# Kernel tuning notes

Measured on AMD Instinct MI355X. Metric: run time of the kernel, lower is better.

The kernel has to match this reference:

```python
import jax, jax.numpy as jnp
import numpy as np

B, T, F, H, M = 64, 512, 32, 512, 20
O = (F + 2) * M  # (n_features + 2) * num_mixtures = 680


def _lstm_cell(x, h, c, w_ih, w_hh, b_ih, b_hh):
    # torch.nn.LSTMCell: gates ordered [i, f, g, o]
    gates = x @ w_ih.T + h @ w_hh.T + b_ih + b_hh
    i, f, g, o = jnp.split(gates, 4, axis=-1)
    i = jax.nn.sigmoid(i)
    f = jax.nn.sigmoid(f)
    g = jnp.tanh(g)
    o = jax.nn.sigmoid(o)
    c_new = f * c + i * g
    h_new = o * jnp.tanh(c_new)
    return h_new, c_new


def setup_inputs() -> dict:
    key = jax.random.key(0)
    ks = jax.random.split(key, 9)
    s1 = 1.0 / np.sqrt(H)  # torch LSTMCell init: U(-1/sqrt(hidden), 1/sqrt(hidden))
    s2 = 1.0 / np.sqrt(O)
    u = lambda k, shape, s: jax.random.uniform(k, shape, jnp.float32, -s, s)
    return {
        "data": jax.random.normal(ks[0], (B, T * F), jnp.float32),
        "W_ih1": u(ks[1], (4 * H, F), s1),
        "W_hh1": u(ks[2], (4 * H, H), s1),
        "b_ih1": u(ks[3], (4 * H,), s1),
        "b_hh1": u(ks[4], (4 * H,), s1),
        "W_ih2": u(ks[5], (4 * O, H), s2),
        "W_hh2": u(ks[6], (4 * O, O), s2),
        "b_ih2": u(ks[7], (4 * O,), s2),
        "b_hh2": u(ks[8], (4 * O,), s2),
    }


def reference(data, W_ih1, W_hh1, b_ih1, b_hh1, W_ih2, W_hh2, b_ih2, b_hh2):
    n_feat = W_ih1.shape[1]
    hid = W_hh1.shape[1]
    out_dim = W_hh2.shape[1]
    batch = data.shape[0]
    t_steps = data.shape[1] // n_feat
    xs = data.reshape(batch, t_steps, n_feat).transpose(1, 0, 2)  # (T, B, F)

    h1 = jnp.zeros((batch, hid), data.dtype)
    c1 = jnp.zeros((batch, hid), data.dtype)
    h2 = jnp.zeros((batch, out_dim), data.dtype)
    c2 = jnp.zeros((batch, out_dim), data.dtype)

    def step(carry, x_t):
        h1, c1, h2, c2 = carry
        h1, c1 = _lstm_cell(x_t, h1, c1, W_ih1, W_hh1, b_ih1, b_hh1)
        # NOTE: original feeds lstm1's CELL state c1 into lstm2, and collects
        # lstm2's CELL state (`output`) as the per-step output.
        h2, c2 = _lstm_cell(c1, h2, c2, W_ih2, W_hh2, b_ih2, b_hh2)
        return (h1, c1, h2, c2), c2

    _, outs = jax.lax.scan(step, (h1, c1, h2, c2), xs)  # (T, B, O)
    return outs.transpose(1, 0, 2)  # (B, T, O), matches torch.stack(outputs, 1)
```

## Files before the change

### kernel.cpp

```cpp
#include <hip/hip_runtime.h>
#include <math.h>

#define BB 64
#define TT 512
#define FF 32
#define HH 512
#define OO 680

typedef _Float16 half8 __attribute__((ext_vector_type(8)));
typedef float f32x4 __attribute__((ext_vector_type(4)));

#define H1SLAB 65536u
#define C1SLAB 65536u
#define H2SLAB 90112u
#define H1S_OFF 0u
#define C1S_OFF 131072u
#define H2S_OFF 393216u
#define BAR_OFF 573440u
#define MEMSET_BYTES 576000u

#define L1B  16
#define NBLK 59
#define LDS_BYTES 155648u

#define L1CNT(g) ((g)*32)
#define L1FLG    64
#define L2CNT(g) (96 + (g)*32)
#define L2FLG    352

__device__ __forceinline__ float sigf(float x) { return 1.f / (1.f + expf(-x)); }

__device__ __forceinline__ unsigned long long aload8(const void* p) {
    return __hip_atomic_load((const unsigned long long*)p, __ATOMIC_RELAXED, __HIP_MEMORY_SCOPE_AGENT);
}
__device__ __forceinline__ void astore8(void* p, unsigned long long v) {
    __hip_atomic_store((unsigned long long*)p, v, __ATOMIC_RELAXED, __HIP_MEMORY_SCOPE_AGENT);
}
__device__ __forceinline__ void astore32(unsigned* p, unsigned v) {
    __hip_atomic_store(p, v, __ATOMIC_RELAXED, __HIP_MEMORY_SCOPE_AGENT);
}
__device__ __forceinline__ half8 ld_act(const char* p) {
    union { unsigned long long u[2]; half8 h; } t;
    t.u[0] = aload8(p); t.u[1] = aload8(p + 8);
    return t.h;
}
__device__ __forceinline__ unsigned pack2h(float a, float b) {
    union { _Float16 h[2]; unsigned u; } t;
    t.h[0] = (_Float16)a; t.h[1] = (_Float16)b; return t.u;
}
__device__ __forceinline__ unsigned long long pack4h(float a, float b, float c, float d) {
    union { _Float16 h[4]; unsigned long long u; } t;
    t.h[0] = (_Float16)a; t.h[1] = (_Float16)b; t.h[2] = (_Float16)c; t.h[3] = (_Float16)d;
    return t.u;
}
__device__ __forceinline__ unsigned minL1(const unsigned* bar) {
    const unsigned long long v = aload8(bar + L1FLG);
    const unsigned a = (unsigned)v, b = (unsigned)(v >> 32);
    return a < b ? a : b;
}
__device__ __forceinline__ unsigned minL2(const unsigned* bar) {
    const unsigned long long v0 = aload8(bar + L2FLG);
    const unsigned long long v1 = aload8(bar + L2FLG + 2);
    const unsigned long long v2 = aload8(bar + L2FLG + 4);
    const unsigned long long v3 = aload8(bar + L2FLG + 6);
    unsigned m = (unsigned)v0;
    unsigned x;
    x = (unsigned)(v0 >> 32); m = x < m ? x : m;
    x = (unsigned)v1;         m = x < m ? x : m;
    x = (unsigned)(v1 >> 32); m = x < m ? x : m;
    x = (unsigned)v2;         m = x < m ? x : m;
    x = (unsigned)(v2 >> 32); m = x < m ? x : m;
    x = (unsigned)v3;         m = x < m ? x : m;
    x = (unsigned)(v3 >> 32); m = x < m ? x : m;
    return m;
}

__global__ __launch_bounds__(256, 1)
void rnn_mfma(const float* __restrict__ data,
    const float* __restrict__ Wih1, const float* __restrict__ Whh1,
    const float* __restrict__ bih1, const float* __restrict__ bhh1,
    const float* __restrict__ Wih2, const float* __restrict__ Whh2,
    const float* __restrict__ bih2, const float* __restrict__ bhh2,
    char* __restrict__ wsb, float* __restrict__ out)
{
    extern __shared__ char lds[];
    const int tid = threadIdx.x, wv = tid >> 6, l = tid & 63;
    const int hi = l >> 4, lo = l & 15;
    const int blk = blockIdx.x;
    unsigned* bar = (unsigned*)(wsb + BAR_OFF);
    const int bfrag = wv;
    const int b = bfrag * 16 + lo;

    if (blk < L1B) {
        const int c0 = blk * 32;
        for (int u = tid; u < 136 * 256; u += 256) {
            const int tile = u >> 8, w = u & 255;
            const int ll = w >> 2, jj = w & 3;
            const int ks = tile >> 3, rest = tile & 7;
            const int gate = rest >> 1, chi = rest & 1;
            const int col = c0 + chi * 16 + (ll & 15);
            const int row = gate * HH + col;
            const int kk = ks * 32 + (ll >> 4) * 8 + jj * 2;
            const float v0 = (kk < FF)     ? Wih1[(size_t)row * FF + kk]     : Whh1[(size_t)row * HH + kk - FF];
            const float v1 = (kk + 1 < FF) ? Wih1[(size_t)row * FF + kk + 1] : Whh1[(size_t)row * HH + kk + 1 - FF];
            ((unsigned*)lds)[tile * 256 + w] = pack2h(v0, v1);
        }
        __syncthreads();

        float bs[2][4][4];
        #pragma unroll
        for (int chi = 0; chi < 2; ++chi)
            #pragma unroll
            for (int r = 0; r < 4; ++r) {
                const int col = c0 + chi * 16 + hi * 4 + r;
                #pragma unroll
                for (int g = 0; g < 4; ++g)
                    bs[chi][r][g] = bih1[g * HH + col] + bhh1[g * HH + col];
            }
        float cr[8] = {0.f,0.f,0.f,0.f,0.f,0.f,0.f,0.f};

        for (int s = 0; s < TT; ++s) {
            const int pr = s & 1;
            const float* xp = data + (size_t)b * (TT * FF) + (size_t)s * FF + hi * 8;
            const float4 xa = *(const float4*)xp;
            const float4 xb4 = *(const float4*)(xp + 4);
            if (s > 0) {
                if (tid == 0) { while (minL1(bar) < (unsigned)s) {} }
                __syncthreads();
            }
            half8 bx;
            bx[0] = (_Float16)xa.x; bx[1] = (_Float16)xa.y; bx[2] = (_Float16)xa.z; bx[3] = (_Float16)xa.w;
            bx[4] = (_Float16)xb4.x; bx[5] = (_Float16)xb4.y; bx[6] = (_Float16)xb4.z; bx[7] = (_Float16)xb4.w;

            f32x4 acc[8];
            #pragma unroll
            for (int a = 0; a < 8; ++a) acc[a] = (f32x4){0.f,0.f,0.f,0.f};
            #pragma unroll
            for (int a = 0; a < 8; ++a)
                acc[a] = __builtin_amdgcn_mfma_f32_16x16x32_f16(*(const half8*)(lds + (size_t)a * 1024 + (size_t)l * 16), bx, acc[a], 0, 0, 0);
            const char* h1p = wsb + H1S_OFF + (size_t)pr * H1SLAB + (size_t)l * 16;
            #pragma unroll
            for (int ks = 1; ks <= 16; ++ks) {
                const half8 bf = ld_act(h1p + (size_t)((ks - 1) * 4 + bfrag) * 1024);
                #pragma unroll
                for (int a = 0; a < 8; ++a)
                    acc[a] = __builtin_amdgcn_mfma_f32_16x16x32_f16(*(const half8*)(lds + (size_t)(ks * 8 + a) * 1024 + (size_t)l * 16), bf, acc[a], 0, 0, 0);
            }
            if (s > 3) {
                if (tid == 0) { while (minL2(bar) < (unsigned)(s - 3)) {} }
                __syncthreads();
            }
            char* h1w = wsb + H1S_OFF + (size_t)(pr ^ 1) * H1SLAB;
            char* c1w = wsb + C1S_OFF + (size_t)(s & 3) * C1SLAB;
            #pragma unroll
            for (int chi = 0; chi < 2; ++chi) {
                const int cc = c0 + chi * 16 + hi * 4;
                float cn[4], hn[4];
                #pragma unroll
                for (int r = 0; r < 4; ++r) {
                    const float ig = sigf(acc[0 + chi][r] + bs[chi][r][0]);
                    const float fg = sigf(acc[2 + chi][r] + bs[chi][r][1]);
                    const float gg = tanhf(acc[4 + chi][r] + bs[chi][r][2]);
                    const float og = sigf(acc[6 + chi][r] + bs[chi][r][3]);
                    const float c = fg * cr[chi * 4 + r] + ig * gg;
                    cr[chi * 4 + r] = c;
                    cn[r] = c; hn[r] = og * tanhf(c);
                }
                const size_t aoff = (size_t)((cc >> 5) * 4 + bfrag) * 1024
                                  + (size_t)((((cc >> 3) & 3) * 16 + lo)) * 16
                                  + (size_t)(cc & 7) * 2;
                astore8(h1w + aoff, pack4h(hn[0], hn[1], hn[2], hn[3]));
                astore8(c1w + aoff, pack4h(cn[0], cn[1], cn[2], cn[3]));
            }
            __syncthreads();
            if (tid == 0) {
                const int g = blk & 1;
                const unsigned e = (unsigned)(s + 1);
                const unsigned a2 = __hip_atomic_fetch_add(bar + L1CNT(g), 1u, __ATOMIC_RELAXED, __HIP_MEMORY_SCOPE_AGENT);
                if (a2 == e * 8u - 1u) astore32(bar + L1FLG + g, e);
            }
        }
    } else {
        const int idx = blk - L1B, c0 = idx * 16;
        const int grp = idx & 7;
        const unsigned gsz = (grp < 3) ? 6u : 5u;
        for (int u = tid; u < 152 * 256; u += 256) {
            const int tile = u >> 8, w = u & 255;
            const int ll = w >> 2, jj = w & 3;
            const int ks = tile >> 2, gate = tile & 3;
            const int col = c0 + (ll & 15);
            const int kk = ks * 32 + (ll >> 4) * 8 + jj * 2;
            float v0 = 0.f, v1 = 0.f;
            if (col < OO) {
                if (kk < HH) v0 = Wih2[((size_t)gate * OO + col) * HH + kk];
                else if (kk < 1192) v0 = Whh2[((size_t)gate * OO + col) * OO + kk - HH];
                if (kk + 1 < HH) v1 = Wih2[((size_t)gate * OO + col) * HH + kk + 1];
                else if (kk + 1 < 1192) v1 = Whh2[((size_t)gate * OO + col) * OO + kk + 1 - HH];
            }
            ((unsigned*)lds)[tile * 256 + w] = pack2h(v0, v1);
        }
        __syncthreads();

        const int cc = c0 + hi * 4;
        float bs[4][4];
        #pragma unroll
        for (int r = 0; r < 4; ++r) {
            const int col = cc + r;
            const bool ok = col < OO;
            #pragma unroll
            for (int g = 0; g < 4; ++g)
                bs[r][g] = ok ? (bih2[g * OO + col] + bhh2[g * OO + col]) : 0.f;
        }
        float cr[4] = {0.f,0.f,0.f,0.f};

        for (int t = 1; t <= TT; ++t) {
            if (tid == 0) { while (minL1(bar) < (unsigned)t) {} }
            __syncthreads();
            const char* c1p = wsb + C1S_OFF + (size_t)((t - 1) & 3) * C1SLAB + (size_t)l * 16;
            half8 bcs[16];
            #pragma unroll
            for (int ks = 0; ks < 16; ++ks) bcs[ks] = ld_act(c1p + (size_t)(ks * 4 + bfrag) * 1024);
            if (t > 1) {
                if (tid == 0) { while (minL2(bar) < (unsigned)(t - 1)) {} }
                __syncthreads();
            }
            const char* h2p = wsb + H2S_OFF + (size_t)((t & 1) ^ 1) * H2SLAB + (size_t)l * 16;
            half8 bhs[22];
            #pragma unroll
            for (int ks = 0; ks < 22; ++ks) bhs[ks] = ld_act(h2p + (size_t)(ks * 4 + bfrag) * 1024);
            f32x4 acc[4];
            #pragma unroll
            for (int g = 0; g < 4; ++g) acc[g] = (f32x4){0.f,0.f,0.f,0.f};
            #pragma unroll
            for (int ks = 0; ks < 16; ++ks) {
                #pragma unroll
                for (int g = 0; g < 4; ++g)
                    acc[g] = __builtin_amdgcn_mfma_f32_16x16x32_f16(*(const half8*)(lds + (size_t)(ks * 4 + g) * 1024 + (size_t)l * 16), bcs[ks], acc[g], 0, 0, 0);
            }
            #pragma unroll
            for (int ks = 0; ks < 22; ++ks) {
                #pragma unroll
                for (int g = 0; g < 4; ++g)
                    acc[g] = __builtin_amdgcn_mfma_f32_16x16x32_f16(*(const half8*)(lds + (size_t)((16 + ks) * 4 + g) * 1024 + (size_t)l * 16), bhs[ks], acc[g], 0, 0, 0);
            }
            if (cc < OO) {
                const int u_ = t - 1;
                float cn[4], hn[4];
                #pragma unroll
                for (int r = 0; r < 4; ++r) {
                    const float ig = sigf(acc[0][r] + bs[r][0]);
                    const float fg = sigf(acc[1][r] + bs[r][1]);
                    const float gg = tanhf(acc[2][r] + bs[r][2]);
                    const float og = sigf(acc[3][r] + bs[r][3]);
                    const float c = fg * cr[r] + ig * gg;
                    cr[r] = c;
                    cn[r] = c; hn[r] = og * tanhf(c);
                }
                const f32x4 q = {cn[0], cn[1], cn[2], cn[3]};
                __builtin_nontemporal_store(q, (f32x4*)(out + (size_t)b * (TT * OO) + (size_t)u_ * OO + cc));
                char* h2w = wsb + H2S_OFF + (size_t)(t & 1) * H2SLAB;
                const size_t aoff = (size_t)((cc >> 5) * 4 + bfrag) * 1024
                                  + (size_t)((((cc >> 3) & 3) * 16 + lo)) * 16
                                  + (size_t)(cc & 7) * 2;
                astore8(h2w + aoff, pack4h(hn[0], hn[1], hn[2], hn[3]));
            }
            __syncthreads();
            if (t < TT && tid == 0) {
                const unsigned a2 = __hip_atomic_fetch_add(bar + L2CNT(grp), 1u, __ATOMIC_RELAXED, __HIP_MEMORY_SCOPE_AGENT);
                if (a2 == (unsigned)t * gsz - 1u) astore32(bar + L2FLG + grp, (unsigned)t);
            }
        }
    }
}

extern "C" void kernel_launch(void* const* d_in, const int* in_sizes, int n_in,
                              void* d_out, int out_size, void* d_ws, size_t ws_size,
                              hipStream_t stream)
{
    const float* data = (const float*)d_in[0];
    const float* Wih1 = (const float*)d_in[1];
    const float* Whh1 = (const float*)d_in[2];
    const float* bih1 = (const float*)d_in[3];
    const float* bhh1 = (const float*)d_in[4];
    const float* Wih2 = (const float*)d_in[5];
    const float* Whh2 = (const float*)d_in[6];
    const float* bih2 = (const float*)d_in[7];
    const float* bhh2 = (const float*)d_in[8];
    float* out = (float*)d_out;
    char* wsb  = (char*)d_ws;

    hipFuncSetAttribute((const void*)rnn_mfma, hipFuncAttributeMaxDynamicSharedMemorySize, (int)LDS_BYTES);
    hipMemsetAsync(wsb, 0, MEMSET_BYTES, stream);
    rnn_mfma<<<NBLK, 256, LDS_BYTES, stream>>>(data,
                                               Wih1, Whh1, bih1, bhh1,
                                               Wih2, Whh2, bih2, bhh2,
                                               wsb, out);
}
```

Baseline: 4.495 ms.

## Replace block-level flag barriers with per-wave counter polling and overlap input MFMAs

Each wave now bumps a per-group counter after its own stores drain, replacing the __syncthreads plus block-leader fetch-add that also published a group flag. Every wave polls all counters itself with s_sleep backoff, so no block-wide barrier is needed. The input-projection MFMAs (x for layer 1, c1 for layer 2) are moved ahead of the dependency waits so they overlap the wait. This removes per-step block barriers and one level of flag indirection, at the cost of more polling traffic from every wave and a reliance on relaxed atomics plus waitcnt for ordering.

```diff
diff --git a/kernel.cpp b/kernel.cpp
--- a/kernel.cpp
+++ b/kernel.cpp
@@ -24,20 +24,18 @@
 #define LDS_BYTES 155648u
 
 #define L1CNT(g) ((g)*32)
-#define L1FLG    64
-#define L2CNT(g) (96 + (g)*32)
-#define L2FLG    352
+#define L2CNT(g) (64 + (g)*32)
 
 __device__ __forceinline__ float sigf(float x) { return 1.f / (1.f + expf(-x)); }
 
+__device__ __forceinline__ unsigned al32(const unsigned* p) {
+    return __hip_atomic_load(p, __ATOMIC_RELAXED, __HIP_MEMORY_SCOPE_AGENT);
+}
 __device__ __forceinline__ unsigned long long aload8(const void* p) {
     return __hip_atomic_load((const unsigned long long*)p, __ATOMIC_RELAXED, __HIP_MEMORY_SCOPE_AGENT);
 }
 __device__ __forceinline__ void astore8(void* p, unsigned long long v) {
     __hip_atomic_store((unsigned long long*)p, v, __ATOMIC_RELAXED, __HIP_MEMORY_SCOPE_AGENT);
-}
-__device__ __forceinline__ void astore32(unsigned* p, unsigned v) {
-    __hip_atomic_store(p, v, __ATOMIC_RELAXED, __HIP_MEMORY_SCOPE_AGENT);
 }
 __device__ __forceinline__ half8 ld_act(const char* p) {
     union { unsigned long long u[2]; half8 h; } t;
@@ -53,26 +51,25 @@
     t.h[0] = (_Float16)a; t.h[1] = (_Float16)b; t.h[2] = (_Float16)c; t.h[3] = (_Float16)d;
     return t.u;
 }
-__device__ __forceinline__ unsigned minL1(const unsigned* bar) {
-    const unsigned long long v = aload8(bar + L1FLG);
-    const unsigned a = (unsigned)v, b = (unsigned)(v >> 32);
-    return a < b ? a : b;
-}
-__device__ __forceinline__ unsigned minL2(const unsigned* bar) {
-    const unsigned long long v0 = aload8(bar + L2FLG);
-    const unsigned long long v1 = aload8(bar + L2FLG + 2);
-    const unsigned long long v2 = aload8(bar + L2FLG + 4);
-    const unsigned long long v3 = aload8(bar + L2FLG + 6);
-    unsigned m = (unsigned)v0;
-    unsigned x;
-    x = (unsigned)(v0 >> 32); m = x < m ? x : m;
-    x = (unsigned)v1;         m = x < m ? x : m;
-    x = (unsigned)(v1 >> 32); m = x < m ? x : m;
-    x = (unsigned)v2;         m = x < m ? x : m;
-    x = (unsigned)(v2 >> 32); m = x < m ? x : m;
-    x = (unsigned)v3;         m = x < m ? x : m;
-    x = (unsigned)(v3 >> 32); m = x < m ? x : m;
-    return m;
+
+__device__ __forceinline__ void wait2_ge(const unsigned* p0, const unsigned* p1, unsigned tgt) {
+    for (;;) {
+        const unsigned a = al32(p0), b = al32(p1);
+        if (a >= tgt && b >= tgt) return;
+        __builtin_amdgcn_s_sleep(1);
+    }
+}
+__device__ __forceinline__ bool l2done(const unsigned* bar, unsigned e) {
+    unsigned ok = 1u;
+    ok &= (al32(bar + L2CNT(0)) >= e * 24u);
+    ok &= (al32(bar + L2CNT(1)) >= e * 24u);
+    ok &= (al32(bar + L2CNT(2)) >= e * 24u);
+    ok &= (al32(bar + L2CNT(3)) >= e * 20u);
+    ok &= (al32(bar + L2CNT(4)) >= e * 20u);
+    ok &= (al32(bar + L2CNT(5)) >= e * 20u);
+    ok &= (al32(bar + L2CNT(6)) >= e * 20u);
+    ok &= (al32(bar + L2CNT(7)) >= e * 20u);
+    return ok != 0u;
 }
 
 __global__ __launch_bounds__(256, 1)
@@ -124,20 +121,18 @@
             const float* xp = data + (size_t)b * (TT * FF) + (size_t)s * FF + hi * 8;
             const float4 xa = *(const float4*)xp;
             const float4 xb4 = *(const float4*)(xp + 4);
-            if (s > 0) {
-                if (tid == 0) { while (minL1(bar) < (unsigned)s) {} }
-                __syncthreads();
-            }
             half8 bx;
             bx[0] = (_Float16)xa.x; bx[1] = (_Float16)xa.y; bx[2] = (_Float16)xa.z; bx[3] = (_Float16)xa.w;
             bx[4] = (_Float16)xb4.x; bx[5] = (_Float16)xb4.y; bx[6] = (_Float16)xb4.z; bx[7] = (_Float16)xb4.w;
-
             f32x4 acc[8];
             #pragma unroll
             for (int a = 0; a < 8; ++a) acc[a] = (f32x4){0.f,0.f,0.f,0.f};
             #pragma unroll
             for (int a = 0; a < 8; ++a)
                 acc[a] = __builtin_amdgcn_mfma_f32_16x16x32_f16(*(const half8*)(lds + (size_t)a * 1024 + (size_t)l * 16), bx, acc[a], 0, 0, 0);
+
+            if (s > 0) wait2_ge(bar + L1CNT(0), bar + L1CNT(1), (unsigned)s * 32u);
+
             const char* h1p = wsb + H1S_OFF + (size_t)pr * H1SLAB + (size_t)l * 16;
             #pragma unroll
             for (int ks = 1; ks <= 16; ++ks) {
@@ -147,8 +142,8 @@
                     acc[a] = __builtin_amdgcn_mfma_f32_16x16x32_f16(*(const half8*)(lds + (size_t)(ks * 8 + a) * 1024 + (size_t)l * 16), bf, acc[a], 0, 0, 0);
             }
             if (s > 3) {
-                if (tid == 0) { while (minL2(bar) < (unsigned)(s - 3)) {} }
-                __syncthreads();
+                const unsigned e = (unsigned)(s - 3);
+                while (!l2done(bar, e)) __builtin_amdgcn_s_sleep(8);
             }
             char* h1w = wsb + H1S_OFF + (size_t)(pr ^ 1) * H1SLAB;
             char* c1w = wsb + C1S_OFF + (size_t)(s & 3) * C1SLAB;
@@ -172,18 +167,13 @@
                 astore8(h1w + aoff, pack4h(hn[0], hn[1], hn[2], hn[3]));
                 astore8(c1w + aoff, pack4h(cn[0], cn[1], cn[2], cn[3]));
             }
-            __syncthreads();
-            if (tid == 0) {
-                const int g = blk & 1;
-                const unsigned e = (unsigned)(s + 1);
-                const unsigned a2 = __hip_atomic_fetch_add(bar + L1CNT(g), 1u, __ATOMIC_RELAXED, __HIP_MEMORY_SCOPE_AGENT);
-                if (a2 == e * 8u - 1u) astore32(bar + L1FLG + g, e);
-            }
+            __builtin_amdgcn_s_waitcnt(0);
+            if (l == 0)
+                __hip_atomic_fetch_add(bar + L1CNT(blk & 1), 1u, __ATOMIC_RELAXED, __HIP_MEMORY_SCOPE_AGENT);
         }
     } else {
         const int idx = blk - L1B, c0 = idx * 16;
         const int grp = idx & 7;
-        const unsigned gsz = (grp < 3) ? 6u : 5u;
         for (int u = tid; u < 152 * 256; u += 256) {
             const int tile = u >> 8, w = u & 255;
             const int ll = w >> 2, jj = w & 3;
@@ -214,29 +204,28 @@
         float cr[4] = {0.f,0.f,0.f,0.f};
 
         for (int t = 1; t <= TT; ++t) {
-            if (tid == 0) { while (minL1(bar) < (unsigned)t) {} }
-            __syncthreads();
+            wait2_ge(bar + L1CNT(0), bar + L1CNT(1), (unsigned)t * 32u);
             const char* c1p = wsb + C1S_OFF + (size_t)((t - 1) & 3) * C1SLAB + (size_t)l * 16;
             half8 bcs[16];
             #pragma unroll
             for (int ks = 0; ks < 16; ++ks) bcs[ks] = ld_act(c1p + (size_t)(ks * 4 + bfrag) * 1024);
-            if (t > 1) {
-                if (tid == 0) { while (minL2(bar) < (unsigned)(t - 1)) {} }
-                __syncthreads();
+            f32x4 acc[4];
+            #pragma unroll
+            for (int g = 0; g < 4; ++g) acc[g] = (f32x4){0.f,0.f,0.f,0.f};
+            #pragma unroll
+            for (int ks = 0; ks < 16; ++ks) {
+                #pragma unroll
+                for (int g = 0; g < 4; ++g)
+                    acc[g] = __builtin_amdgcn_mfma_f32_16x16x32_f16(*(const half8*)(lds + (size_t)(ks * 4 + g) * 1024 + (size_t)l * 16), bcs[ks], acc[g], 0, 0, 0);
+            }
+            {
+                const unsigned e = (unsigned)(t - 1);
+                while (!l2done(bar, e)) __builtin_amdgcn_s_sleep(1);
             }
             const char* h2p = wsb + H2S_OFF + (size_t)((t & 1) ^ 1) * H2SLAB + (size_t)l * 16;
             half8 bhs[22];
             #pragma unroll
             for (int ks = 0; ks < 22; ++ks) bhs[ks] = ld_act(h2p + (size_t)(ks * 4 + bfrag) * 1024);
-            f32x4 acc[4];
-            #pragma unroll
-            for (int g = 0; g < 4; ++g) acc[g] = (f32x4){0.f,0.f,0.f,0.f};
-            #pragma unroll
-            for (int ks = 0; ks < 16; ++ks) {
-                #pragma unroll
-                for (int g = 0; g < 4; ++g)
-                    acc[g] = __builtin_amdgcn_mfma_f32_16x16x32_f16(*(const half8*)(lds + (size_t)(ks * 4 + g) * 1024 + (size_t)l * 16), bcs[ks], acc[g], 0, 0, 0);
-            }
             #pragma unroll
             for (int ks = 0; ks < 22; ++ks) {
                 #pragma unroll
@@ -264,11 +253,9 @@
                                   + (size_t)(cc & 7) * 2;
                 astore8(h2w + aoff, pack4h(hn[0], hn[1], hn[2], hn[3]));
             }
-            __syncthreads();
-            if (t < TT && tid == 0) {
-                const unsigned a2 = __hip_atomic_fetch_add(bar + L2CNT(grp), 1u, __ATOMIC_RELAXED, __HIP_MEMORY_SCOPE_AGENT);
-                if (a2 == (unsigned)t * gsz - 1u) astore32(bar + L2FLG + grp, (unsigned)t);
-            }
+            __builtin_amdgcn_s_waitcnt(0);
+            if (t < TT && l == 0)
+                __hip_atomic_fetch_add(bar + L2CNT(grp), 1u, __ATOMIC_RELAXED, __HIP_MEMORY_SCOPE_AGENT);
         }
     }
 }
```

New measurement: 5.376 ms. +19.6%, slower.

## Merge LSTM1 and LSTM2 into uniform blocks with one shared barrier per step

Applied to the files above, without the earlier changes.

Replaces the split design (16 layer-1 blocks plus 43 layer-2 blocks with separate flags) with 64 identical blocks. Each block owns 8 layer-1 columns and 12 layer-2 columns with gate-interleaved weight tiles, and runs layer-1 step s alongside layer-2 step s-1 under a single grid barrier per step. The aim is to balance work and cut cross-group synchronisation latency on the serial recurrence. The cost is that every block now does both layers' MFMAs each step, and lane shuffles are needed to regroup gate outputs.

```diff
diff --git a/kernel.cpp b/kernel.cpp
--- a/kernel.cpp
+++ b/kernel.cpp
@@ -10,23 +10,18 @@
 typedef _Float16 half8 __attribute__((ext_vector_type(8)));
 typedef float f32x4 __attribute__((ext_vector_type(4)));
 
-#define H1SLAB 65536u
-#define C1SLAB 65536u
-#define H2SLAB 90112u
 #define H1S_OFF 0u
 #define C1S_OFF 131072u
-#define H2S_OFF 393216u
-#define BAR_OFF 573440u
-#define MEMSET_BYTES 576000u
-
-#define L1B  16
-#define NBLK 59
-#define LDS_BYTES 155648u
-
-#define L1CNT(g) ((g)*32)
-#define L1FLG    64
-#define L2CNT(g) (96 + (g)*32)
-#define L2FLG    352
+#define H2S_OFF 262144u
+#define BAR_OFF 442368u
+#define MEMSET_BYTES 443648u
+
+#define NBLK 64
+#define LDS_BYTES 151552u
+#define L2W_OFF 34816u
+
+#define CNT(g) ((g)*32)
+#define FLG    256
 
 __device__ __forceinline__ float sigf(float x) { return 1.f / (1.f + expf(-x)); }
 
@@ -53,18 +48,12 @@
     t.h[0] = (_Float16)a; t.h[1] = (_Float16)b; t.h[2] = (_Float16)c; t.h[3] = (_Float16)d;
     return t.u;
 }
-__device__ __forceinline__ unsigned minL1(const unsigned* bar) {
-    const unsigned long long v = aload8(bar + L1FLG);
-    const unsigned a = (unsigned)v, b = (unsigned)(v >> 32);
-    return a < b ? a : b;
-}
-__device__ __forceinline__ unsigned minL2(const unsigned* bar) {
-    const unsigned long long v0 = aload8(bar + L2FLG);
-    const unsigned long long v1 = aload8(bar + L2FLG + 2);
-    const unsigned long long v2 = aload8(bar + L2FLG + 4);
-    const unsigned long long v3 = aload8(bar + L2FLG + 6);
-    unsigned m = (unsigned)v0;
-    unsigned x;
+__device__ __forceinline__ unsigned minFlag(const unsigned* bar) {
+    const unsigned long long v0 = aload8(bar + FLG);
+    const unsigned long long v1 = aload8(bar + FLG + 2);
+    const unsigned long long v2 = aload8(bar + FLG + 4);
+    const unsigned long long v3 = aload8(bar + FLG + 6);
+    unsigned m = (unsigned)v0, x;
     x = (unsigned)(v0 >> 32); m = x < m ? x : m;
     x = (unsigned)v1;         m = x < m ? x : m;
     x = (unsigned)(v1 >> 32); m = x < m ? x : m;
@@ -74,9 +63,14 @@
     x = (unsigned)(v3 >> 32); m = x < m ? x : m;
     return m;
 }
+__device__ __forceinline__ size_t slab_waddr(int cc, int b) {
+    return (size_t)((cc >> 5) * 4 + (b >> 4)) * 1024
+         + (size_t)((((cc >> 3) & 3) * 16 + (b & 15))) * 16
+         + (size_t)(cc & 7) * 2;
+}
 
 __global__ __launch_bounds__(256, 1)
-void rnn_mfma(const float* __restrict__ data,
+void rnn_merged(const float* __restrict__ data,
     const float* __restrict__ Wih1, const float* __restrict__ Whh1,
     const float* __restrict__ bih1, const float* __restrict__ bhh1,
     const float* __restrict__ Wih2, const float* __restrict__ Whh2,
@@ -86,189 +80,179 @@
     extern __shared__ char lds[];
     const int tid = threadIdx.x, wv = tid >> 6, l = tid & 63;
     const int hi = l >> 4, lo = l & 15;
-    const int blk = blockIdx.x;
+    const int bk = blockIdx.x;
     unsigned* bar = (unsigned*)(wsb + BAR_OFF);
-    const int bfrag = wv;
-    const int b = bfrag * 16 + lo;
-
-    if (blk < L1B) {
-        const int c0 = blk * 32;
-        for (int u = tid; u < 136 * 256; u += 256) {
-            const int tile = u >> 8, w = u & 255;
-            const int ll = w >> 2, jj = w & 3;
-            const int ks = tile >> 3, rest = tile & 7;
-            const int gate = rest >> 1, chi = rest & 1;
-            const int col = c0 + chi * 16 + (ll & 15);
-            const int row = gate * HH + col;
-            const int kk = ks * 32 + (ll >> 4) * 8 + jj * 2;
-            const float v0 = (kk < FF)     ? Wih1[(size_t)row * FF + kk]     : Whh1[(size_t)row * HH + kk - FF];
-            const float v1 = (kk + 1 < FF) ? Wih1[(size_t)row * FF + kk + 1] : Whh1[(size_t)row * HH + kk + 1 - FF];
-            ((unsigned*)lds)[tile * 256 + w] = pack2h(v0, v1);
-        }
-        __syncthreads();
-
-        float bs[2][4][4];
+    const int b = wv * 16 + lo;
+
+    for (int u = tid; u < 34 * 256; u += 256) {
+        const int tt = u >> 8, w = u & 255;
+        const int ks = tt >> 1, q = tt & 1;
+        const int ll = w >> 2, jj = w & 3;
+        const int fq = q * 16 + (ll & 15);
+        const int col = bk * 8 + (fq >> 2);
+        const int gate = fq & 3;
+        const int grow = gate * HH + col;
+        const int k = ks * 32 + (ll >> 4) * 8 + jj * 2;
+        const float v0 = (k < FF)     ? Wih1[(size_t)grow * FF + k]     : Whh1[(size_t)grow * HH + k - FF];
+        const float v1 = (k + 1 < FF) ? Wih1[(size_t)grow * FF + k + 1] : Whh1[(size_t)grow * HH + k + 1 - FF];
+        ((unsigned*)lds)[tt * 256 + w] = pack2h(v0, v1);
+    }
+    for (int u = tid; u < 114 * 256; u += 256) {
+        const int tt = u >> 8, w = u & 255;
+        const int ks = tt / 3, q = tt - ks * 3;
+        const int ll = w >> 2, jj = w & 3;
+        const int fq = q * 16 + (ll & 15);
+        const int col = bk * 12 + (fq >> 2);
+        const int gate = fq & 3;
+        const int k = ks * 32 + (ll >> 4) * 8 + jj * 2;
+        float v0 = 0.f, v1 = 0.f;
+        if (col < OO) {
+            if (k < HH) v0 = Wih2[((size_t)gate * OO + col) * HH + k];
+            else if (k < 1192) v0 = Whh2[((size_t)gate * OO + col) * OO + k - HH];
+            if (k + 1 < HH) v1 = Wih2[((size_t)gate * OO + col) * HH + k + 1];
+            else if (k + 1 < 1192) v1 = Whh2[((size_t)gate * OO + col) * OO + k + 1 - HH];
+        }
+        ((unsigned*)(lds + L2W_OFF))[tt * 256 + w] = pack2h(v0, v1);
+    }
+    __syncthreads();
+
+    float bs1[2][4], bs2[3][4];
+    #pragma unroll
+    for (int q = 0; q < 2; ++q) {
+        const int col = bk * 8 + q * 4 + hi;
         #pragma unroll
-        for (int chi = 0; chi < 2; ++chi)
-            #pragma unroll
-            for (int r = 0; r < 4; ++r) {
-                const int col = c0 + chi * 16 + hi * 4 + r;
-                #pragma unroll
-                for (int g = 0; g < 4; ++g)
-                    bs[chi][r][g] = bih1[g * HH + col] + bhh1[g * HH + col];
-            }
-        float cr[8] = {0.f,0.f,0.f,0.f,0.f,0.f,0.f,0.f};
-
-        for (int s = 0; s < TT; ++s) {
-            const int pr = s & 1;
+        for (int g = 0; g < 4; ++g) bs1[q][g] = bih1[g * HH + col] + bhh1[g * HH + col];
+    }
+    #pragma unroll
+    for (int q = 0; q < 3; ++q) {
+        const int col = bk * 12 + q * 4 + hi;
+        const bool ok = col < OO;
+        #pragma unroll
+        for (int g = 0; g < 4; ++g) bs2[q][g] = ok ? (bih2[g * OO + col] + bhh2[g * OO + col]) : 0.f;
+    }
+    float cr1[2] = {0.f, 0.f};
+    float cr2[3] = {0.f, 0.f, 0.f};
+
+    for (int s = 0; s <= TT; ++s) {
+        const int wr = s & 1, rd = wr ^ 1;
+        f32x4 a10 = {0,0,0,0}, a11 = {0,0,0,0};
+        if (s < TT) {
             const float* xp = data + (size_t)b * (TT * FF) + (size_t)s * FF + hi * 8;
             const float4 xa = *(const float4*)xp;
             const float4 xb4 = *(const float4*)(xp + 4);
-            if (s > 0) {
-                if (tid == 0) { while (minL1(bar) < (unsigned)s) {} }
-                __syncthreads();
-            }
             half8 bx;
             bx[0] = (_Float16)xa.x; bx[1] = (_Float16)xa.y; bx[2] = (_Float16)xa.z; bx[3] = (_Float16)xa.w;
             bx[4] = (_Float16)xb4.x; bx[5] = (_Float16)xb4.y; bx[6] = (_Float16)xb4.z; bx[7] = (_Float16)xb4.w;
-
-            f32x4 acc[8];
-            #pragma unroll
-            for (int a = 0; a < 8; ++a) acc[a] = (f32x4){0.f,0.f,0.f,0.f};
-            #pragma unroll
-            for (int a = 0; a < 8; ++a)
-                acc[a] = __builtin_amdgcn_mfma_f32_16x16x32_f16(*(const half8*)(lds + (size_t)a * 1024 + (size_t)l * 16), bx, acc[a], 0, 0, 0);
-            const char* h1p = wsb + H1S_OFF + (size_t)pr * H1SLAB + (size_t)l * 16;
+            a10 = __builtin_amdgcn_mfma_f32_16x16x32_f16(*(const half8*)(lds + (size_t)l * 16), bx, a10, 0, 0, 0);
+            a11 = __builtin_amdgcn_mfma_f32_16x16x32_f16(*(const half8*)(lds + 1024 + (size_t)l * 16), bx, a11, 0, 0, 0);
+        }
+        if (s > 0) {
+            if (tid == 0) { while (minFlag(bar) < (unsigned)s) {} }
+            __syncthreads();
+        }
+        float pend[4]; float* pendP = nullptr;
+
+        if (s < TT) {
+            const char* h1p = wsb + H1S_OFF + (size_t)rd * 65536u + (size_t)l * 16;
+            half8 bh[16];
+            #pragma unroll
+            for (int ks = 0; ks < 16; ++ks) bh[ks] = ld_act(h1p + (size_t)(ks * 4 + wv) * 1024);
             #pragma unroll
             for (int ks = 1; ks <= 16; ++ks) {
-                const half8 bf = ld_act(h1p + (size_t)((ks - 1) * 4 + bfrag) * 1024);
-                #pragma unroll
-                for (int a = 0; a < 8; ++a)
-                    acc[a] = __builtin_amdgcn_mfma_f32_16x16x32_f16(*(const half8*)(lds + (size_t)(ks * 8 + a) * 1024 + (size_t)l * 16), bf, acc[a], 0, 0, 0);
-            }
-            if (s > 3) {
-                if (tid == 0) { while (minL2(bar) < (unsigned)(s - 3)) {} }
-                __syncthreads();
-            }
-            char* h1w = wsb + H1S_OFF + (size_t)(pr ^ 1) * H1SLAB;
-            char* c1w = wsb + C1S_OFF + (size_t)(s & 3) * C1SLAB;
-            #pragma unroll
-            for (int chi = 0; chi < 2; ++chi) {
-                const int cc = c0 + chi * 16 + hi * 4;
-                float cn[4], hn[4];
-                #pragma unroll
-                for (int r = 0; r < 4; ++r) {
-                    const float ig = sigf(acc[0 + chi][r] + bs[chi][r][0]);
-                    const float fg = sigf(acc[2 + chi][r] + bs[chi][r][1]);
-                    const float gg = tanhf(acc[4 + chi][r] + bs[chi][r][2]);
-                    const float og = sigf(acc[6 + chi][r] + bs[chi][r][3]);
-                    const float c = fg * cr[chi * 4 + r] + ig * gg;
-                    cr[chi * 4 + r] = c;
-                    cn[r] = c; hn[r] = og * tanhf(c);
+                a10 = __builtin_amdgcn_mfma_f32_16x16x32_f16(*(const half8*)(lds + (size_t)(ks * 2) * 1024 + (size_t)l * 16), bh[ks - 1], a10, 0, 0, 0);
+                a11 = __builtin_amdgcn_mfma_f32_16x16x32_f16(*(const half8*)(lds + (size_t)(ks * 2 + 1) * 1024 + (size_t)l * 16), bh[ks - 1], a11, 0, 0, 0);
+            }
+            float cn1[2], hn1[2];
+            #pragma unroll
+            for (int q = 0; q < 2; ++q) {
+                const f32x4 a = (q == 0) ? a10 : a11;
+                const float ig = sigf(a[0] + bs1[q][0]);
+                const float fg = sigf(a[1] + bs1[q][1]);
+                const float gg = tanhf(a[2] + bs1[q][2]);
+                const float og = sigf(a[3] + bs1[q][3]);
+                const float c = fg * cr1[q] + ig * gg;
+                cr1[q] = c;
+                cn1[q] = c; hn1[q] = og * tanhf(c);
+            }
+            char* h1w = wsb + H1S_OFF + (size_t)wr * 65536u;
+            char* c1w = wsb + C1S_OFF + (size_t)wr * 65536u;
+            #pragma unroll
+            for (int q = 0; q < 2; ++q) {
+                const float h0 = __shfl(hn1[q], lo), h1v = __shfl(hn1[q], 16 + lo);
+                const float h2v = __shfl(hn1[q], 32 + lo), h3 = __shfl(hn1[q], 48 + lo);
+                const float c0 = __shfl(cn1[q], lo), c1v = __shfl(cn1[q], 16 + lo);
+                const float c2v = __shfl(cn1[q], 32 + lo), c3 = __shfl(cn1[q], 48 + lo);
+                if (hi == q) {
+                    const int cc = bk * 8 + q * 4;
+                    const size_t ad = slab_waddr(cc, b);
+                    astore8(h1w + ad, pack4h(h0, h1v, h2v, h3));
+                    astore8(c1w + ad, pack4h(c0, c1v, c2v, c3));
                 }
-                const size_t aoff = (size_t)((cc >> 5) * 4 + bfrag) * 1024
-                                  + (size_t)((((cc >> 3) & 3) * 16 + lo)) * 16
-                                  + (size_t)(cc & 7) * 2;
-                astore8(h1w + aoff, pack4h(hn[0], hn[1], hn[2], hn[3]));
-                astore8(c1w + aoff, pack4h(cn[0], cn[1], cn[2], cn[3]));
-            }
-            __syncthreads();
-            if (tid == 0) {
-                const int g = blk & 1;
-                const unsigned e = (unsigned)(s + 1);
-                const unsigned a2 = __hip_atomic_fetch_add(bar + L1CNT(g), 1u, __ATOMIC_RELAXED, __HIP_MEMORY_SCOPE_AGENT);
-                if (a2 == e * 8u - 1u) astore32(bar + L1FLG + g, e);
-            }
-        }
-    } else {
-        const int idx = blk - L1B, c0 = idx * 16;
-        const int grp = idx & 7;
-        const unsigned gsz = (grp < 3) ? 6u : 5u;
-        for (int u = tid; u < 152 * 256; u += 256) {
-            const int tile = u >> 8, w = u & 255;
-            const int ll = w >> 2, jj = w & 3;
-            const int ks = tile >> 2, gate = tile & 3;
-            const int col = c0 + (ll & 15);
-            const int kk = ks * 32 + (ll >> 4) * 8 + jj * 2;
-            float v0 = 0.f, v1 = 0.f;
-            if (col < OO) {
-                if (kk < HH) v0 = Wih2[((size_t)gate * OO + col) * HH + kk];
-                else if (kk < 1192) v0 = Whh2[((size_t)gate * OO + col) * OO + kk - HH];
-                if (kk + 1 < HH) v1 = Wih2[((size_t)gate * OO + col) * HH + kk + 1];
-                else if (kk + 1 < 1192) v1 = Whh2[((size_t)gate * OO + col) * OO + kk + 1 - HH];
-            }
-            ((unsigned*)lds)[tile * 256 + w] = pack2h(v0, v1);
+            }
+        }
+        if (s >= 1) {
+            f32x4 a20 = {0,0,0,0}, a21 = {0,0,0,0}, a22 = {0,0,0,0};
+            const char* c1p = wsb + C1S_OFF + (size_t)rd * 65536u + (size_t)l * 16;
+            half8 bc[16];
+            #pragma unroll
+            for (int ks = 0; ks < 16; ++ks) bc[ks] = ld_act(c1p + (size_t)(ks * 4 + wv) * 1024);
+            #pragma unroll
+            for (int ks = 0; ks < 16; ++ks) {
+                const char* at = lds + L2W_OFF + (size_t)(ks * 3) * 1024 + (size_t)l * 16;
+                a20 = __builtin_amdgcn_mfma_f32_16x16x32_f16(*(const half8*)(at       ), bc[ks], a20, 0, 0, 0);
+                a21 = __builtin_amdgcn_mfma_f32_16x16x32_f16(*(const half8*)(at + 1024), bc[ks], a21, 0, 0, 0);
+                a22 = __builtin_amdgcn_mfma_f32_16x16x32_f16(*(const half8*)(at + 2048), bc[ks], a22, 0, 0, 0);
+            }
+            const char* h2p = wsb + H2S_OFF + (size_t)rd * 90112u + (size_t)l * 16;
+            half8 bh2[22];
+            #pragma unroll
+            for (int kk = 0; kk < 22; ++kk) bh2[kk] = ld_act(h2p + (size_t)(kk * 4 + wv) * 1024);
+            #pragma unroll
+            for (int kk = 0; kk < 22; ++kk) {
+                const char* at = lds + L2W_OFF + (size_t)((16 + kk) * 3) * 1024 + (size_t)l * 16;
+                a20 = __builtin_amdgcn_mfma_f32_16x16x32_f16(*(const half8*)(at       ), bh2[kk], a20, 0, 0, 0);
+                a21 = __builtin_amdgcn_mfma_f32_16x16x32_f16(*(const half8*)(at + 1024), bh2[kk], a21, 0, 0, 0);
+                a22 = __builtin_amdgcn_mfma_f32_16x16x32_f16(*(const half8*)(at + 2048), bh2[kk], a22, 0, 0, 0);
+            }
+            float cn2[3], hn2[3];
+            #pragma unroll
+            for (int q = 0; q < 3; ++q) {
+                const f32x4 a = (q == 0) ? a20 : (q == 1) ? a21 : a22;
+                const float ig = sigf(a[0] + bs2[q][0]);
+                const float fg = sigf(a[1] + bs2[q][1]);
+                const float gg = tanhf(a[2] + bs2[q][2]);
+                const float og = sigf(a[3] + bs2[q][3]);
+                const float c = fg * cr2[q] + ig * gg;
+                cr2[q] = c;
+                cn2[q] = c; hn2[q] = og * tanhf(c);
+            }
+            char* h2w = wsb + H2S_OFF + (size_t)wr * 90112u;
+            #pragma unroll
+            for (int q = 0; q < 3; ++q) {
+                const float h0 = __shfl(hn2[q], lo), h1v = __shfl(hn2[q], 16 + lo);
+                const float h2v = __shfl(hn2[q], 32 + lo), h3 = __shfl(hn2[q], 48 + lo);
+                const float c0 = __shfl(cn2[q], lo), c1v = __shfl(cn2[q], 16 + lo);
+                const float c2v = __shfl(cn2[q], 32 + lo), c3 = __shfl(cn2[q], 48 + lo);
+                if (hi == q) {
+                    const int cc = bk * 12 + q * 4;
+                    if (cc + 4 <= OO) {
+                        astore8(h2w + slab_waddr(cc, b), pack4h(h0, h1v, h2v, h3));
+                        pend[0] = c0; pend[1] = c1v; pend[2] = c2v; pend[3] = c3;
+                        pendP = out + (size_t)b * (TT * OO) + (size_t)(s - 1) * OO + cc;
+                    }
+                }
+            }
         }
         __syncthreads();
-
-        const int cc = c0 + hi * 4;
-        float bs[4][4];
-        #pragma unroll
-        for (int r = 0; r < 4; ++r) {
-            const int col = cc + r;
-            const bool ok = col < OO;
-            #pragma unroll
-            for (int g = 0; g < 4; ++g)
-                bs[r][g] = ok ? (bih2[g * OO + col] + bhh2[g * OO + col]) : 0.f;
-        }
-        float cr[4] = {0.f,0.f,0.f,0.f};
-
-        for (int t = 1; t <= TT; ++t) {
-            if (tid == 0) { while (minL1(bar) < (unsigned)t) {} }
-            __syncthreads();
-            const char* c1p = wsb + C1S_OFF + (size_t)((t - 1) & 3) * C1SLAB + (size_t)l * 16;
-            half8 bcs[16];
-            #pragma unroll
-            for (int ks = 0; ks < 16; ++ks) bcs[ks] = ld_act(c1p + (size_t)(ks * 4 + bfrag) * 1024);
-            if (t > 1) {
-                if (tid == 0) { while (minL2(bar) < (unsigned)(t - 1)) {} }
-                __syncthreads();
-            }
-            const char* h2p = wsb + H2S_OFF + (size_t)((t & 1) ^ 1) * H2SLAB + (size_t)l * 16;
-            half8 bhs[22];
-            #pragma unroll
-            for (int ks = 0; ks < 22; ++ks) bhs[ks] = ld_act(h2p + (size_t)(ks * 4 + bfrag) * 1024);
-            f32x4 acc[4];
-            #pragma unroll
-            for (int g = 0; g < 4; ++g) acc[g] = (f32x4){0.f,0.f,0.f,0.f};
-            #pragma unroll
-            for (int ks = 0; ks < 16; ++ks) {
-                #pragma unroll
-                for (int g = 0; g < 4; ++g)
-                    acc[g] = __builtin_amdgcn_mfma_f32_16x16x32_f16(*(const half8*)(lds + (size_t)(ks * 4 + g) * 1024 + (size_t)l * 16), bcs[ks], acc[g], 0, 0, 0);
-            }
-            #pragma unroll
-            for (int ks = 0; ks < 22; ++ks) {
-                #pragma unroll
-                for (int g = 0; g < 4; ++g)
-                    acc[g] = __builtin_amdgcn_mfma_f32_16x16x32_f16(*(const half8*)(lds + (size_t)((16 + ks) * 4 + g) * 1024 + (size_t)l * 16), bhs[ks], acc[g], 0, 0, 0);
-            }
-            if (cc < OO) {
-                const int u_ = t - 1;
-                float cn[4], hn[4];
-                #pragma unroll
-                for (int r = 0; r < 4; ++r) {
-                    const float ig = sigf(acc[0][r] + bs[r][0]);
-                    const float fg = sigf(acc[1][r] + bs[r][1]);
-                    const float gg = tanhf(acc[2][r] + bs[r][2]);
-                    const float og = sigf(acc[3][r] + bs[r][3]);
-                    const float c = fg * cr[r] + ig * gg;
-                    cr[r] = c;
-                    cn[r] = c; hn[r] = og * tanhf(c);
-                }
-                const f32x4 q = {cn[0], cn[1], cn[2], cn[3]};
-                __builtin_nontemporal_store(q, (f32x4*)(out + (size_t)b * (TT * OO) + (size_t)u_ * OO + cc));
-                char* h2w = wsb + H2S_OFF + (size_t)(t & 1) * H2SLAB;
-                const size_t aoff = (size_t)((cc >> 5) * 4 + bfrag) * 1024
-                                  + (size_t)((((cc >> 3) & 3) * 16 + lo)) * 16
-                                  + (size_t)(cc & 7) * 2;
-                astore8(h2w + aoff, pack4h(hn[0], hn[1], hn[2], hn[3]));
-            }
-            __syncthreads();
-            if (t < TT && tid == 0) {
-                const unsigned a2 = __hip_atomic_fetch_add(bar + L2CNT(grp), 1u, __ATOMIC_RELAXED, __HIP_MEMORY_SCOPE_AGENT);
-                if (a2 == (unsigned)t * gsz - 1u) astore32(bar + L2FLG + grp, (unsigned)t);
-            }
+        if (s < TT && tid == 0) {
+            const int g = bk & 7;
+            const unsigned e = (unsigned)(s + 1);
+            const unsigned a = __hip_atomic_fetch_add(bar + CNT(g), 1u, __ATOMIC_RELAXED, __HIP_MEMORY_SCOPE_AGENT);
+            if (a == e * 8u - 1u) astore32(bar + FLG + g, e);
+        }
+        if (pendP) {
+            const f32x4 q4 = {pend[0], pend[1], pend[2], pend[3]};
+            __builtin_nontemporal_store(q4, (f32x4*)pendP);
         }
     }
 }
@@ -289,10 +273,10 @@
     float* out = (float*)d_out;
     char* wsb  = (char*)d_ws;
 
-    hipFuncSetAttribute((const void*)rnn_mfma, hipFuncAttributeMaxDynamicSharedMemorySize, (int)LDS_BYTES);
+    hipFuncSetAttribute((const void*)rnn_merged, hipFuncAttributeMaxDynamicSharedMemorySize, (int)LDS_BYTES);
     hipMemsetAsync(wsb, 0, MEMSET_BYTES, stream);
-    rnn_mfma<<<NBLK, 256, LDS_BYTES, stream>>>(data,
-                                               Wih1, Whh1, bih1, bhh1,
-                                               Wih2, Whh2, bih2, bhh2,
-                                               wsb, out);
-}
+    rnn_merged<<<NBLK, 256, LDS_BYTES, stream>>>(data,
+                                                 Wih1, Whh1, bih1, bhh1,
+                                                 Wih2, Whh2, bih2, bhh2,
+                                                 wsb, out);
+}
```

New measurement: 4.211 ms. 1.07x faster.
